# Kernel optimization log

Hardware: AMD Instinct MI355X
Metric: run time of the kernel (lower is better)

## Reference

```python
import jax, jax.numpy as jnp
import numpy as np

N = 16384          # points
DIM = 256          # feature dim
HEADS = 8
HD = DIM // HEADS  # head dim = 32
K = 20             # neighbors
MLP_HID = int(DIM * 4.0)
CHUNK = 2048       # query chunk for kNN (avoids N^2 matrix)
EPS = 1e-5
SCALE = HD ** -0.5


def layernorm(x, w, b):
    m = jnp.mean(x, axis=-1, keepdims=True)
    v = jnp.var(x, axis=-1, keepdims=True)
    return (x - m) * jax.lax.rsqrt(v + EPS) * w + b


def knn_graph(positions):
    """Brute-force kNN (squared L2) computed in query chunks. [N, K] indices, self excluded."""
    def chunk_fn(q):  # q: [CHUNK, 3]
        d = jnp.sum((q[:, None, :] - positions[None, :, :]) ** 2, axis=-1)  # [CHUNK, N]
        _, idx = jax.lax.top_k(-d, K + 1)  # ascending distance; first col is self (dist 0)
        return idx[:, 1:]
    idx = jax.lax.map(chunk_fn, positions.reshape(-1, CHUNK, 3))
    return idx.reshape(-1, K)


def setup_inputs() -> dict:
    key = jax.random.key(0)
    ks = jax.random.split(key, 10)
    w = lambda k, s: jax.random.normal(k, s, jnp.float32) * 0.02
    return {
        "x": jax.random.normal(ks[0], (N, DIM), jnp.float32),
        "positions": jax.random.normal(ks[1], (N, 3), jnp.float32),
        "ln1_w": jnp.ones((DIM,), jnp.float32), "ln1_b": jnp.zeros((DIM,), jnp.float32),
        "Wq": w(ks[2], (DIM, DIM)), "bq": jnp.zeros((DIM,), jnp.float32),
        "Wk": w(ks[3], (DIM, DIM)), "bk": jnp.zeros((DIM,), jnp.float32),
        "Wv": w(ks[4], (DIM, DIM)), "bv": jnp.zeros((DIM,), jnp.float32),
        "Wo": w(ks[5], (DIM, DIM)), "bo": jnp.zeros((DIM,), jnp.float32),
        "ln2_w": jnp.ones((DIM,), jnp.float32), "ln2_b": jnp.zeros((DIM,), jnp.float32),
        "W1": w(ks[6], (MLP_HID, DIM)), "b1": jnp.zeros((MLP_HID,), jnp.float32),
        "W2": w(ks[7], (DIM, MLP_HID)), "b2": jnp.zeros((DIM,), jnp.float32),
    }


def reference(x, positions, ln1_w, ln1_b, Wq, bq, Wk, bk, Wv, bv, Wo, bo,
              ln2_w, ln2_b, W1, b1, W2, b2):
    knn = knn_graph(positions)                      # [N, K] int32
    h = layernorm(x, ln1_w, ln1_b)                  # [N, D]
    q = (h @ Wq.T + bq).reshape(N, HEADS, HD)       # [N, H, hd]
    k = h @ Wk.T + bk                               # [N, D]
    v = h @ Wv.T + bv
    kn = k[knn].reshape(N, K, HEADS, HD)            # gather neighbor keys   [N, K, H, hd]
    vn = v[knn].reshape(N, K, HEADS, HD)            # gather neighbor values
    scores = jnp.einsum('nhd,nkhd->nhk', q, kn) * SCALE  # [N, H, K]
    attn = jax.nn.softmax(scores, axis=-1)
    out = jnp.einsum('nhk,nkhd->nhd', attn, vn).reshape(N, DIM)
    x = x + out @ Wo.T + bo                          # residual 1
    h2 = layernorm(x, ln2_w, ln2_b)
    mlp = jax.nn.gelu(h2 @ W1.T + b1, approximate=False) @ W2.T + b2
    return x + mlp                                   # residual 2
```

## Files before the change

kernel.cpp:

```cpp
#include <hip/hip_runtime.h>
#include <math.h>

#define N_PTS 16384
#define DIMS 256
#define HEADS 8
#define HDIM 32
#define KNN 20
#define MLPH 1024
#define SCALE 0.17677669529663687f

typedef unsigned short u16;
typedef unsigned long long ull;
typedef __attribute__((ext_vector_type(8))) short bf16x8;
typedef __attribute__((ext_vector_type(8))) unsigned short u16x8;
typedef __attribute__((ext_vector_type(4))) float f32x4;

__device__ __forceinline__ float bf2f(u16 u) {
  return __uint_as_float(((unsigned int)u) << 16);
}
__device__ __forceinline__ u16 f2bf(float f) {
  unsigned int u = __float_as_uint(f);
  u += 0x7fffu + ((u >> 16) & 1u);
  return (u16)(u >> 16);
}
__device__ __forceinline__ float fin(float v) {
  return __builtin_isfinite(v) ? v : 0.f;
}
__device__ __forceinline__ float dist2(float4 a, float4 b) {
  float dx = a.x - b.x, dy = a.y - b.y, dz = a.z - b.z;
  return dx * dx + dy * dy + dz * dz;
}
__device__ __forceinline__ u16x8 cvt8(float4 a, float4 b) {
  u16x8 o;
  o[0] = f2bf(a.x); o[1] = f2bf(a.y); o[2] = f2bf(a.z); o[3] = f2bf(a.w);
  o[4] = f2bf(b.x); o[5] = f2bf(b.y); o[6] = f2bf(b.z); o[7] = f2bf(b.w);
  return o;
}


__global__ __launch_bounds__(256) void knn_init(const float* __restrict__ pos,
                                                float4* __restrict__ pos4,
                                                int* __restrict__ cnt,
                                                int* __restrict__ nbr) {
  int i = blockIdx.x * 256 + threadIdx.x;
  cnt[i] = 0;
#pragma unroll
  for (int j = 0; j < KNN; ++j) nbr[i * KNN + j] = 0;
  float x = fin(pos[3 * i]), y = fin(pos[3 * i + 1]), z = fin(pos[3 * i + 2]);
  pos4[i] = make_float4(x, y, z, x * x + y * y + z * z);
}


__global__ __launch_bounds__(256) void knn_shardmin(const float4* __restrict__ pos4,
                                                    float* __restrict__ Mmin) {
  __shared__ float4 cp[256];
  int shard = blockIdx.x;
  int qbase = blockIdx.y * 1024 + threadIdx.x;
  cp[threadIdx.x] = pos4[shard * 256 + threadIdx.x];
  float m2x[4], m2y[4], m2z[4], mn[4];
#pragma unroll
  for (int k = 0; k < 4; ++k) {
    float4 qp = pos4[qbase + k * 256];
    m2x[k] = -2.f * qp.x; m2y[k] = -2.f * qp.y; m2z[k] = -2.f * qp.z;
    mn[k] = 3.4e38f;
  }
  __syncthreads();
#pragma unroll 4
  for (int c = 0; c < 256; ++c) {
    float4 cc = cp[c];
#pragma unroll
    for (int k = 0; k < 4; ++k) {
      float t = fmaf(m2z[k], cc.z, cc.w);
      t = fmaf(m2y[k], cc.y, t);
      t = fmaf(m2x[k], cc.x, t);
      mn[k] = fminf(mn[k], t);
    }
  }
#pragma unroll
  for (int k = 0; k < 4; ++k) Mmin[shard * N_PTS + qbase + k * 256] = mn[k];
}

__global__ __launch_bounds__(256) void knn_tau(const float* __restrict__ Mmin,
                                               float* __restrict__ tau) {
  int q = blockIdx.x * 256 + threadIdx.x;
  float a[21];
#pragma unroll
  for (int j = 0; j < 21; ++j) a[j] = 3.4e38f;
  for (int s = 0; s < 64; ++s) {
    float v = Mmin[s * N_PTS + q];
    a[20] = fminf(a[20], v);
#pragma unroll
    for (int j = 20; j >= 1; --j) {
      float lo = fminf(a[j - 1], a[j]), hi = fmaxf(a[j - 1], a[j]);
      a[j - 1] = lo; a[j] = hi;
    }
  }
  tau[q] = a[20];
}

__global__ __launch_bounds__(256) void knn_collect(const float4* __restrict__ pos4,
                                                   const float* __restrict__ tau,
                                                   int* __restrict__ cnt,
                                                   ull* __restrict__ surv) {
  __shared__ float4 cp[256];
  int cbase = blockIdx.x * 256;
  int qbase = blockIdx.y * 1024 + threadIdx.x;
  cp[threadIdx.x] = pos4[cbase + threadIdx.x];
  float4 qp[4];
  float m2x[4], m2y[4], m2z[4], tq[4];
  unsigned int packed[4];
  int hitcnt[4];
#pragma unroll
  for (int k = 0; k < 4; ++k) {
    qp[k] = pos4[qbase + k * 256];
    m2x[k] = -2.f * qp[k].x; m2y[k] = -2.f * qp[k].y; m2z[k] = -2.f * qp[k].z;
    tq[k] = tau[qbase + k * 256] + 2e-4f;
    packed[k] = 0; hitcnt[k] = 0;
  }
  __syncthreads();
#pragma unroll 4
  for (int c = 0; c < 256; ++c) {
    float4 cc = cp[c];
#pragma unroll
    for (int k = 0; k < 4; ++k) {
      float t = fmaf(m2z[k], cc.z, cc.w);
      t = fmaf(m2y[k], cc.y, t);
      t = fmaf(m2x[k], cc.x, t);
      bool hit = (t <= tq[k]);
      packed[k] = hit ? ((packed[k] << 8) | (unsigned)c) : packed[k];
      hitcnt[k] += hit ? 1 : 0;
    }
  }
#pragma unroll
  for (int k = 0; k < 4; ++k) {
    int hc = hitcnt[k];
    if (hc > 0) {
      int q = qbase + k * 256;
      if (hc <= 4) {
        int slot = atomicAdd(&cnt[q], hc);
        for (int i = 0; i < hc; ++i) {
          int c = (packed[k] >> (8 * i)) & 255;
          float d = dist2(qp[k], cp[c]);
          ull key = ((ull)__float_as_uint(d) << 32) | (unsigned)(cbase + c);
          if (slot + i < 128) surv[(size_t)q * 128 + slot + i] = key;
        }
      } else {
        for (int c = 0; c < 256; ++c) {
          float4 cc = cp[c];
          float t = fmaf(m2z[k], cc.z, cc.w);
          t = fmaf(m2y[k], cc.y, t);
          t = fmaf(m2x[k], cc.x, t);
          if (t <= tq[k]) {
            float d = dist2(qp[k], cc);
            ull key = ((ull)__float_as_uint(d) << 32) | (unsigned)(cbase + c);
            int slot = atomicAdd(&cnt[q], 1);
            if (slot < 128) surv[(size_t)q * 128 + slot] = key;
          }
        }
      }
    }
  }
}

__global__ void knn_rank(const int* __restrict__ cnt,
                         const ull* __restrict__ surv,
                         int* __restrict__ nbr) {
  __shared__ ull s[128];
  int q = blockIdx.x;
  int c = min(cnt[q], 128);
  for (int i = threadIdx.x; i < c; i += 64) s[i] = surv[(size_t)q * 128 + i];
  __syncthreads();
  for (int i = threadIdx.x; i < c; i += 64) {
    ull key = s[i];
    int rank = 0;
    for (int j = 0; j < c; ++j) rank += (s[j] < key);
    if (rank >= 1 && rank <= KNN) nbr[q * KNN + rank - 1] = (int)(key & 0xffffffffu);
  }
}


__global__ __launch_bounds__(256) void ln_kernel(const float* __restrict__ xin,
                                                 const float* __restrict__ w,
                                                 const float* __restrict__ b,
                                                 u16* __restrict__ out) {
  int row = blockIdx.x * 4 + (threadIdx.x >> 6);
  int lane = threadIdx.x & 63;
  float4 u = ((const float4*)(xin + row * DIMS))[lane];
  float f[4] = {fin(u.x), fin(u.y), fin(u.z), fin(u.w)};
  float sum = f[0] + f[1] + f[2] + f[3];
  float sq = f[0] * f[0] + f[1] * f[1] + f[2] * f[2] + f[3] * f[3];
#pragma unroll
  for (int o = 32; o > 0; o >>= 1) {
    sum += __shfl_xor(sum, o);
    sq += __shfl_xor(sq, o);
  }
  float mean = sum * (1.f / 256.f);
  float var = fmaxf(sq * (1.f / 256.f) - mean * mean, 0.f);
  float rs = rsqrtf(var + 1e-5f);
  float4 wv = ((const float4*)w)[lane];
  float4 bv = ((const float4*)b)[lane];
  ushort4 o4;
  o4.x = f2bf(fin((f[0] - mean) * rs * wv.x + bv.x));
  o4.y = f2bf(fin((f[1] - mean) * rs * wv.y + bv.y));
  o4.z = f2bf(fin((f[2] - mean) * rs * wv.z + bv.z));
  o4.w = f2bf(fin((f[3] - mean) * rs * wv.w + bv.w));
  ((ushort4*)(out + row * DIMS))[lane] = o4;
}

template <int EPI>
__device__ __forceinline__ void gemm_body(const u16* __restrict__ A,
                                          const float* __restrict__ B,
                                          const float* __restrict__ bias,
                                          const float* __restrict__ res,
                                          void* __restrict__ out,
                                          int m0, int n0, int Nc, int K) {
  __shared__ __align__(16) u16 Asm[128 * 32];
  __shared__ __align__(16) u16 Bsm[128 * 32];
  const int t = threadIdx.x;
  const int w = t >> 6, lane = t & 63;
  const int quad = lane >> 4, mr = lane & 15;
  const int wm = (w >> 1) * 64, wn = (w & 1) * 64;
  const int r = t >> 2, sseg = t & 3;

  f32x4 acc[4][4];
  const f32x4 zero4 = {0.f, 0.f, 0.f, 0.f};
#pragma unroll
  for (int i = 0; i < 4; ++i)
#pragma unroll
    for (int j = 0; j < 4; ++j) acc[i][j] = zero4;

  const u16* Ab = A + (size_t)(m0 + r) * K + sseg * 8;
  const float* Bb = B + (size_t)(n0 + r) * K + sseg * 8;
  u16x8* AsmT = (u16x8*)(Asm + t * 8);
  u16x8* BsmT = (u16x8*)(Bsm + t * 8);

  for (int k0 = 0; k0 < K; k0 += 32) {
    u16x8 a0 = *(const u16x8*)(Ab + k0);
    u16x8 a1 = *(const u16x8*)(Ab + k0 + (size_t)64 * K);
    float4 b0a = *(const float4*)(Bb + k0);
    float4 b0b = *(const float4*)(Bb + k0 + 4);
    float4 b1a = *(const float4*)(Bb + k0 + (size_t)64 * K);
    float4 b1b = *(const float4*)(Bb + k0 + (size_t)64 * K + 4);
    u16x8 b0 = cvt8(b0a, b0b);
    u16x8 b1 = cvt8(b1a, b1b);
    __syncthreads();
    AsmT[0] = a0;
    AsmT[256] = a1;
    BsmT[0] = b0;
    BsmT[256] = b1;
    __syncthreads();
    bf16x8 af[4], bfr[4];
#pragma unroll
    for (int i = 0; i < 4; ++i)
      af[i] = *(const bf16x8*)&Asm[(wm + i * 16 + mr) * 32 + quad * 8];
#pragma unroll
    for (int j = 0; j < 4; ++j)
      bfr[j] = *(const bf16x8*)&Bsm[(wn + j * 16 + mr) * 32 + quad * 8];
#pragma unroll
    for (int i = 0; i < 4; ++i)
#pragma unroll
      for (int j = 0; j < 4; ++j)
        acc[i][j] = __builtin_amdgcn_mfma_f32_16x16x32_bf16(af[i], bfr[j], acc[i][j], 0, 0, 0);
  }

  float* outf = (float*)out;
  u16* outb = (u16*)out;
#pragma unroll
  for (int j = 0; j < 4; ++j) {
    int n = n0 + wn + j * 16 + mr;
    float bv = bias[n];
#pragma unroll
    for (int i = 0; i < 4; ++i) {
      int mb = m0 + wm + i * 16 + quad * 4;
#pragma unroll
      for (int rr = 0; rr < 4; ++rr) {
        size_t off = (size_t)(mb + rr) * Nc + n;
        float v = acc[i][j][rr] + bv;
        if (EPI == 0) {
          outb[off] = f2bf(fin(v));
        } else if (EPI == 1) {
          outf[off] = fin(v + res[off]);
        } else {
          float g = 0.5f * v * (1.0f + erff(v * 0.70710678118654752f));
          outb[off] = f2bf(fin(g));
        }
      }
    }
  }
}

template <int EPI>
__global__ __launch_bounds__(256) void gemm_bt(const u16* __restrict__ A,
                                               const float* __restrict__ B,
                                               const float* __restrict__ bias,
                                               const float* __restrict__ res,
                                               void* __restrict__ out,
                                               int Nc, int K) {
  gemm_body<EPI>(A, B, bias, res, out, blockIdx.y * 128, blockIdx.x * 128, Nc, K);
}

__global__ __launch_bounds__(256) void gemm_qkv(const u16* __restrict__ A,
                                                const float* __restrict__ Wq,
                                                const float* __restrict__ Wk,
                                                const float* __restrict__ Wv,
                                                const float* __restrict__ bq,
                                                const float* __restrict__ bk,
                                                const float* __restrict__ bv,
                                                u16* __restrict__ qo,
                                                u16* __restrict__ ko,
                                                u16* __restrict__ vo) {
  int sel = blockIdx.x >> 1;
  const float* B = (sel == 0) ? Wq : ((sel == 1) ? Wk : Wv);
  const float* bias = (sel == 0) ? bq : ((sel == 1) ? bk : bv);
  u16* out = (sel == 0) ? qo : ((sel == 1) ? ko : vo);
  gemm_body<0>(A, B, bias, nullptr, out, blockIdx.y * 128, (blockIdx.x & 1) * 128,
               DIMS, DIMS);
}


__global__ __launch_bounds__(256) void attn_kernel(const u16* __restrict__ Q,
                                                   const u16* __restrict__ Kb,
                                                   const u16* __restrict__ Vb,
                                                   const int* __restrict__ nbr,
                                                   u16* __restrict__ out) {
  int t = blockIdx.x * 256 + threadIdx.x;
  int p = t >> 3, h = t & 7;
  const u16* qrow = Q + (size_t)p * DIMS + h * HDIM;
  float qf[32];
#pragma unroll
  for (int c = 0; c < 4; ++c) {
    u16x8 u = *(const u16x8*)(qrow + c * 8);
#pragma unroll
    for (int e = 0; e < 8; ++e) qf[c * 8 + e] = bf2f(u[e]);
  }
  int idx[KNN];
#pragma unroll
  for (int j = 0; j < KNN; ++j) {
    int ix = nbr[p * KNN + j];
    idx[j] = (ix < 0 || ix >= N_PTS) ? 0 : ix;
  }
  float sc[KNN];
#pragma unroll
  for (int j = 0; j < KNN; ++j) {
    const u16* kr = Kb + (size_t)idx[j] * DIMS + h * HDIM;
    float acc = 0.f;
#pragma unroll
    for (int c = 0; c < 4; ++c) {
      u16x8 u = *(const u16x8*)(kr + c * 8);
#pragma unroll
      for (int e = 0; e < 8; ++e) acc += qf[c * 8 + e] * bf2f(u[e]);
    }
    sc[j] = fin(acc * SCALE);
  }
  float mx = sc[0];
#pragma unroll
  for (int j = 1; j < KNN; ++j) mx = fmaxf(mx, sc[j]);
  float sum = 0.f;
#pragma unroll
  for (int j = 0; j < KNN; ++j) {
    sc[j] = expf(sc[j] - mx);
    sum += sc[j];
  }
  float inv = 1.f / fmaxf(sum, 1e-30f);
  float o[32];
#pragma unroll
  for (int d = 0; d < 32; ++d) o[d] = 0.f;
#pragma unroll
  for (int j = 0; j < KNN; ++j) {
    float wgt = sc[j] * inv;
    const u16* vr = Vb + (size_t)idx[j] * DIMS + h * HDIM;
#pragma unroll
    for (int c = 0; c < 4; ++c) {
      u16x8 u = *(const u16x8*)(vr + c * 8);
#pragma unroll
      for (int e = 0; e < 8; ++e) o[c * 8 + e] = fmaf(wgt, bf2f(u[e]), o[c * 8 + e]);
    }
  }
  u16* orow = out + (size_t)p * DIMS + h * HDIM;
#pragma unroll
  for (int c = 0; c < 4; ++c) {
    u16x8 u;
#pragma unroll
    for (int e = 0; e < 8; ++e) u[e] = f2bf(fin(o[c * 8 + e]));
    *(u16x8*)(orow + c * 8) = u;
  }
}

extern "C" void kernel_launch(void* const* d_in, const int* in_sizes, int n_in,
                              void* d_out, int out_size, void* d_ws, size_t ws_size,
                              hipStream_t stream) {
  const float* x = (const float*)d_in[0];
  const float* positions = (const float*)d_in[1];
  const float* ln1_w = (const float*)d_in[2];
  const float* ln1_b = (const float*)d_in[3];
  const float* Wq = (const float*)d_in[4];
  const float* bq = (const float*)d_in[5];
  const float* Wk = (const float*)d_in[6];
  const float* bk = (const float*)d_in[7];
  const float* Wv = (const float*)d_in[8];
  const float* bv = (const float*)d_in[9];
  const float* Wo = (const float*)d_in[10];
  const float* bo = (const float*)d_in[11];
  const float* ln2_w = (const float*)d_in[12];
  const float* ln2_b = (const float*)d_in[13];
  const float* W1 = (const float*)d_in[14];
  const float* b1 = (const float*)d_in[15];
  const float* W2 = (const float*)d_in[16];
  const float* b2 = (const float*)d_in[17];

  char* w = (char*)d_ws;
  float* x1f = (float*)(w + 0);
  u16* hid = (u16*)(w + 16777216);
  u16* h2 = (u16*)(w + 50331648);
  float4* pos4 = (float4*)(w + 16777216);
  float* Mmin = (float*)(w + 17039360);
  float* tau = (float*)(w + 21233664);
  int* cnt = (int*)(w + 21299200);
  ull* surv = (ull*)(w + 21364736);
  int* nbr = (int*)(w + 38141952);
  u16* h = (u16*)(w + 39452672);
  u16* qb = (u16*)(w + 0);
  u16* kb = (u16*)(w + 8388608);
  u16* vb = (u16*)(w + 21364736);
  u16* ao = (u16*)(w + 29753344);

  knn_init<<<dim3(N_PTS / 256), dim3(256), 0, stream>>>(positions, pos4, cnt, nbr);
  knn_shardmin<<<dim3(64, 16), dim3(256), 0, stream>>>(pos4, Mmin);
  knn_tau<<<dim3(64), dim3(256), 0, stream>>>(Mmin, tau);
  knn_collect<<<dim3(64, 16), dim3(256), 0, stream>>>(pos4, tau, cnt, surv);
  knn_rank<<<dim3(N_PTS), dim3(64), 0, stream>>>(cnt, surv, nbr);

  ln_kernel<<<dim3(N_PTS / 4), dim3(256), 0, stream>>>(x, ln1_w, ln1_b, h);
  gemm_qkv<<<dim3(6, 128), dim3(256), 0, stream>>>(h, Wq, Wk, Wv, bq, bk, bv,
                                                   qb, kb, vb);

  attn_kernel<<<dim3(N_PTS * HEADS / 256), dim3(256), 0, stream>>>(qb, kb, vb, nbr, ao);
  gemm_bt<1><<<dim3(2, 128), dim3(256), 0, stream>>>(ao, Wo, bo, x, x1f, DIMS, DIMS);

  ln_kernel<<<dim3(N_PTS / 4), dim3(256), 0, stream>>>(x1f, ln2_w, ln2_b, h2);
  gemm_bt<2><<<dim3(8, 128), dim3(256), 0, stream>>>(h2, W1, b1, nullptr, hid, MLPH, DIMS);
  gemm_bt<1><<<dim3(2, 128), dim3(256), 0, stream>>>(hid, W2, b2, x1f, (float*)d_out, DIMS, MLPH);
}
```

Measured before the change: 378.4 us.

## Pre-convert attention weights to bf16, use direct-to-LDS loads, reshard kNN

A new kernel converts Wq, Wk, Wv and Wo to bf16 once per call, so the QKV and output-projection GEMMs can stage both operands straight into LDS with global_load_lds and skip per-tile fp32-to-bf16 conversion. The A operand in every GEMM now also uses direct-to-LDS loads. The kNN prefilter switches to 128 shards of 128 candidates, which tightens the tau threshold, and survivor slots drop from 128 to 64 to cut storage and ranking work. The cost is an extra launch, a workspace re-layout, and a risk of overflowing survivor slots if more than 64 candidates pass the threshold.

```diff
diff --git a/kernel.cpp b/kernel.cpp
--- a/kernel.cpp
+++ b/kernel.cpp
@@ -7,6 +7,9 @@
 #define HDIM 32
 #define KNN 20
 #define MLPH 1024
+#define NSHARD 128
+#define SHARDC 128
+#define SURV_SLOTS 64
 #define SCALE 0.17677669529663687f
 
 typedef unsigned short u16;
@@ -35,6 +38,11 @@
   o[0] = f2bf(a.x); o[1] = f2bf(a.y); o[2] = f2bf(a.z); o[3] = f2bf(a.w);
   o[4] = f2bf(b.x); o[5] = f2bf(b.y); o[6] = f2bf(b.z); o[7] = f2bf(b.w);
   return o;
+}
+__device__ __forceinline__ void gld16(const u16* g, u16* l) {
+  __builtin_amdgcn_global_load_lds(
+      (const __attribute__((address_space(1))) unsigned int*)g,
+      (__attribute__((address_space(3))) unsigned int*)l, 16, 0, 0);
 }
 
 
@@ -51,12 +59,27 @@
 }
 
 
+__global__ __launch_bounds__(256) void conv_w(const float* __restrict__ Wq,
+                                              const float* __restrict__ Wk,
+                                              const float* __restrict__ Wv,
+                                              const float* __restrict__ Wo,
+                                              u16* __restrict__ wbf) {
+  int idx = blockIdx.x * 256 + threadIdx.x;
+  int mat = idx >> 14, loc = idx & 16383;
+  const float* src = (mat == 0) ? Wq : ((mat == 1) ? Wk : ((mat == 2) ? Wv : Wo));
+  float4 v = ((const float4*)src)[loc];
+  ushort4 o;
+  o.x = f2bf(v.x); o.y = f2bf(v.y); o.z = f2bf(v.z); o.w = f2bf(v.w);
+  ((ushort4*)(wbf + mat * 65536))[loc] = o;
+}
+
+
 __global__ __launch_bounds__(256) void knn_shardmin(const float4* __restrict__ pos4,
                                                     float* __restrict__ Mmin) {
-  __shared__ float4 cp[256];
+  __shared__ float4 cp[SHARDC];
   int shard = blockIdx.x;
   int qbase = blockIdx.y * 1024 + threadIdx.x;
-  cp[threadIdx.x] = pos4[shard * 256 + threadIdx.x];
+  if (threadIdx.x < SHARDC) cp[threadIdx.x] = pos4[shard * SHARDC + threadIdx.x];
   float m2x[4], m2y[4], m2z[4], mn[4];
 #pragma unroll
   for (int k = 0; k < 4; ++k) {
@@ -66,7 +89,7 @@
   }
   __syncthreads();
 #pragma unroll 4
-  for (int c = 0; c < 256; ++c) {
+  for (int c = 0; c < SHARDC; ++c) {
     float4 cc = cp[c];
 #pragma unroll
     for (int k = 0; k < 4; ++k) {
@@ -86,7 +109,7 @@
   float a[21];
 #pragma unroll
   for (int j = 0; j < 21; ++j) a[j] = 3.4e38f;
-  for (int s = 0; s < 64; ++s) {
+  for (int s = 0; s < NSHARD; ++s) {
     float v = Mmin[s * N_PTS + q];
     a[20] = fminf(a[20], v);
 #pragma unroll
@@ -102,10 +125,10 @@
                                                    const float* __restrict__ tau,
                                                    int* __restrict__ cnt,
                                                    ull* __restrict__ surv) {
-  __shared__ float4 cp[256];
-  int cbase = blockIdx.x * 256;
+  __shared__ float4 cp[SHARDC];
+  int cbase = blockIdx.x * SHARDC;
   int qbase = blockIdx.y * 1024 + threadIdx.x;
-  cp[threadIdx.x] = pos4[cbase + threadIdx.x];
+  if (threadIdx.x < SHARDC) cp[threadIdx.x] = pos4[cbase + threadIdx.x];
   float4 qp[4];
   float m2x[4], m2y[4], m2z[4], tq[4];
   unsigned int packed[4];
@@ -119,7 +142,7 @@
   }
   __syncthreads();
 #pragma unroll 4
-  for (int c = 0; c < 256; ++c) {
+  for (int c = 0; c < SHARDC; ++c) {
     float4 cc = cp[c];
 #pragma unroll
     for (int k = 0; k < 4; ++k) {
@@ -142,10 +165,11 @@
           int c = (packed[k] >> (8 * i)) & 255;
           float d = dist2(qp[k], cp[c]);
           ull key = ((ull)__float_as_uint(d) << 32) | (unsigned)(cbase + c);
-          if (slot + i < 128) surv[(size_t)q * 128 + slot + i] = key;
+          if (slot + i < SURV_SLOTS)
+            surv[(size_t)q * SURV_SLOTS + slot + i] = key;
         }
       } else {
-        for (int c = 0; c < 256; ++c) {
+        for (int c = 0; c < SHARDC; ++c) {
           float4 cc = cp[c];
           float t = fmaf(m2z[k], cc.z, cc.w);
           t = fmaf(m2y[k], cc.y, t);
@@ -154,7 +178,7 @@
             float d = dist2(qp[k], cc);
             ull key = ((ull)__float_as_uint(d) << 32) | (unsigned)(cbase + c);
             int slot = atomicAdd(&cnt[q], 1);
-            if (slot < 128) surv[(size_t)q * 128 + slot] = key;
+            if (slot < SURV_SLOTS) surv[(size_t)q * SURV_SLOTS + slot] = key;
           }
         }
       }
@@ -165,10 +189,10 @@
 __global__ void knn_rank(const int* __restrict__ cnt,
                          const ull* __restrict__ surv,
                          int* __restrict__ nbr) {
-  __shared__ ull s[128];
+  __shared__ ull s[SURV_SLOTS];
   int q = blockIdx.x;
-  int c = min(cnt[q], 128);
-  for (int i = threadIdx.x; i < c; i += 64) s[i] = surv[(size_t)q * 128 + i];
+  int c = min(cnt[q], SURV_SLOTS);
+  for (int i = threadIdx.x; i < c; i += 64) s[i] = surv[(size_t)q * SURV_SLOTS + i];
   __syncthreads();
   for (int i = threadIdx.x; i < c; i += 64) {
     ull key = s[i];
@@ -207,9 +231,9 @@
   ((ushort4*)(out + row * DIMS))[lane] = o4;
 }
 
-template <int EPI>
+template <int EPI, int BW>
 __device__ __forceinline__ void gemm_body(const u16* __restrict__ A,
-                                          const float* __restrict__ B,
+                                          const void* __restrict__ B,
                                           const float* __restrict__ bias,
                                           const float* __restrict__ res,
                                           void* __restrict__ out,
@@ -230,25 +254,33 @@
     for (int j = 0; j < 4; ++j) acc[i][j] = zero4;
 
   const u16* Ab = A + (size_t)(m0 + r) * K + sseg * 8;
-  const float* Bb = B + (size_t)(n0 + r) * K + sseg * 8;
-  u16x8* AsmT = (u16x8*)(Asm + t * 8);
-  u16x8* BsmT = (u16x8*)(Bsm + t * 8);
+  const u16* Bb16 = (const u16*)B + (size_t)(n0 + r) * K + sseg * 8;
+  const float* Bb32 = (const float*)B + (size_t)(n0 + r) * K + sseg * 8;
+  u16* AsmT = Asm + t * 8;
+  u16* BsmT = Bsm + t * 8;
 
   for (int k0 = 0; k0 < K; k0 += 32) {
-    u16x8 a0 = *(const u16x8*)(Ab + k0);
-    u16x8 a1 = *(const u16x8*)(Ab + k0 + (size_t)64 * K);
-    float4 b0a = *(const float4*)(Bb + k0);
-    float4 b0b = *(const float4*)(Bb + k0 + 4);
-    float4 b1a = *(const float4*)(Bb + k0 + (size_t)64 * K);
-    float4 b1b = *(const float4*)(Bb + k0 + (size_t)64 * K + 4);
-    u16x8 b0 = cvt8(b0a, b0b);
-    u16x8 b1 = cvt8(b1a, b1b);
-    __syncthreads();
-    AsmT[0] = a0;
-    AsmT[256] = a1;
-    BsmT[0] = b0;
-    BsmT[256] = b1;
-    __syncthreads();
+    if (BW) {
+      __syncthreads();
+      gld16(Ab + k0, AsmT);
+      gld16(Ab + k0 + (size_t)64 * K, AsmT + 2048);
+      gld16(Bb16 + k0, BsmT);
+      gld16(Bb16 + k0 + (size_t)64 * K, BsmT + 2048);
+      __syncthreads();
+    } else {
+      float4 b0a = *(const float4*)(Bb32 + k0);
+      float4 b0b = *(const float4*)(Bb32 + k0 + 4);
+      float4 b1a = *(const float4*)(Bb32 + k0 + (size_t)64 * K);
+      float4 b1b = *(const float4*)(Bb32 + k0 + (size_t)64 * K + 4);
+      u16x8 b0 = cvt8(b0a, b0b);
+      u16x8 b1 = cvt8(b1a, b1b);
+      __syncthreads();
+      gld16(Ab + k0, AsmT);
+      gld16(Ab + k0 + (size_t)64 * K, AsmT + 2048);
+      *(u16x8*)BsmT = b0;
+      *(u16x8*)(BsmT + 2048) = b1;
+      __syncthreads();
+    }
     bf16x8 af[4], bfr[4];
 #pragma unroll
     for (int i = 0; i < 4; ++i)
@@ -289,20 +321,18 @@
   }
 }
 
-template <int EPI>
+template <int EPI, int BW>
 __global__ __launch_bounds__(256) void gemm_bt(const u16* __restrict__ A,
-                                               const float* __restrict__ B,
+                                               const void* __restrict__ B,
                                                const float* __restrict__ bias,
                                                const float* __restrict__ res,
                                                void* __restrict__ out,
                                                int Nc, int K) {
-  gemm_body<EPI>(A, B, bias, res, out, blockIdx.y * 128, blockIdx.x * 128, Nc, K);
+  gemm_body<EPI, BW>(A, B, bias, res, out, blockIdx.y * 128, blockIdx.x * 128, Nc, K);
 }
 
 __global__ __launch_bounds__(256) void gemm_qkv(const u16* __restrict__ A,
-                                                const float* __restrict__ Wq,
-                                                const float* __restrict__ Wk,
-                                                const float* __restrict__ Wv,
+                                                const u16* __restrict__ wbf,
                                                 const float* __restrict__ bq,
                                                 const float* __restrict__ bk,
                                                 const float* __restrict__ bv,
@@ -310,11 +340,11 @@
                                                 u16* __restrict__ ko,
                                                 u16* __restrict__ vo) {
   int sel = blockIdx.x >> 1;
-  const float* B = (sel == 0) ? Wq : ((sel == 1) ? Wk : Wv);
+  const u16* B = wbf + sel * 65536;
   const float* bias = (sel == 0) ? bq : ((sel == 1) ? bk : bv);
   u16* out = (sel == 0) ? qo : ((sel == 1) ? ko : vo);
-  gemm_body<0>(A, B, bias, nullptr, out, blockIdx.y * 128, (blockIdx.x & 1) * 128,
-               DIMS, DIMS);
+  gemm_body<0, 1>(A, B, bias, nullptr, out, blockIdx.y * 128, (blockIdx.x & 1) * 128,
+                  DIMS, DIMS);
 }
 
 
@@ -409,35 +439,40 @@
   const float* b2 = (const float*)d_in[17];
 
   char* w = (char*)d_ws;
+  const size_t B0 = 16777216;
   float* x1f = (float*)(w + 0);
-  u16* hid = (u16*)(w + 16777216);
+  u16* hid = (u16*)(w + B0);
   u16* h2 = (u16*)(w + 50331648);
-  float4* pos4 = (float4*)(w + 16777216);
-  float* Mmin = (float*)(w + 17039360);
-  float* tau = (float*)(w + 21233664);
-  int* cnt = (int*)(w + 21299200);
-  ull* surv = (ull*)(w + 21364736);
-  int* nbr = (int*)(w + 38141952);
-  u16* h = (u16*)(w + 39452672);
+  float4* pos4 = (float4*)(w + B0);
+  float* Mmin = (float*)(w + B0 + 262144);
+  u16* wbf = (u16*)(w + B0 + 262144);
+  float* tau = (float*)(w + B0 + 8650752);
+  int* cnt = (int*)(w + B0 + 8716288);
+  ull* surv = (ull*)(w + B0 + 8781824);
+  int* nbr = (int*)(w + B0 + 25559040);
+  u16* h = (u16*)(w + B0 + 26869760);
   u16* qb = (u16*)(w + 0);
   u16* kb = (u16*)(w + 8388608);
-  u16* vb = (u16*)(w + 21364736);
-  u16* ao = (u16*)(w + 29753344);
+  u16* vb = (u16*)(w + B0 + 8781824);
+  u16* ao = (u16*)(w + B0 + 17170432);
 
   knn_init<<<dim3(N_PTS / 256), dim3(256), 0, stream>>>(positions, pos4, cnt, nbr);
-  knn_shardmin<<<dim3(64, 16), dim3(256), 0, stream>>>(pos4, Mmin);
+  knn_shardmin<<<dim3(NSHARD, 16), dim3(256), 0, stream>>>(pos4, Mmin);
   knn_tau<<<dim3(64), dim3(256), 0, stream>>>(Mmin, tau);
-  knn_collect<<<dim3(64, 16), dim3(256), 0, stream>>>(pos4, tau, cnt, surv);
+  conv_w<<<dim3(256), dim3(256), 0, stream>>>(Wq, Wk, Wv, Wo, wbf);
+  knn_collect<<<dim3(NSHARD, 16), dim3(256), 0, stream>>>(pos4, tau, cnt, surv);
   knn_rank<<<dim3(N_PTS), dim3(64), 0, stream>>>(cnt, surv, nbr);
 
   ln_kernel<<<dim3(N_PTS / 4), dim3(256), 0, stream>>>(x, ln1_w, ln1_b, h);
-  gemm_qkv<<<dim3(6, 128), dim3(256), 0, stream>>>(h, Wq, Wk, Wv, bq, bk, bv,
-                                                   qb, kb, vb);
+  gemm_qkv<<<dim3(6, 128), dim3(256), 0, stream>>>(h, wbf, bq, bk, bv, qb, kb, vb);
 
   attn_kernel<<<dim3(N_PTS * HEADS / 256), dim3(256), 0, stream>>>(qb, kb, vb, nbr, ao);
-  gemm_bt<1><<<dim3(2, 128), dim3(256), 0, stream>>>(ao, Wo, bo, x, x1f, DIMS, DIMS);
+  gemm_bt<1, 1><<<dim3(2, 128), dim3(256), 0, stream>>>(ao, wbf + 196608, bo, x, x1f,
+                                                        DIMS, DIMS);
 
   ln_kernel<<<dim3(N_PTS / 4), dim3(256), 0, stream>>>(x1f, ln2_w, ln2_b, h2);
-  gemm_bt<2><<<dim3(8, 128), dim3(256), 0, stream>>>(h2, W1, b1, nullptr, hid, MLPH, DIMS);
-  gemm_bt<1><<<dim3(2, 128), dim3(256), 0, stream>>>(hid, W2, b2, x1f, (float*)d_out, DIMS, MLPH);
-}
+  gemm_bt<2, 0><<<dim3(8, 128), dim3(256), 0, stream>>>(h2, W1, b1, nullptr, hid,
+                                                        MLPH, DIMS);
+  gemm_bt<1, 0><<<dim3(2, 128), dim3(256), 0, stream>>>(hid, W2, b2, x1f,
+                                                        (float*)d_out, DIMS, MLPH);
+}
```

Result: no change. 379.6 us (+0.3%).
